# Kernel tuning notes

Hardware: AMD Instinct MI355X
Metric: run time of the kernel (lower is better)

## Reference

```python
import jax, jax.numpy as jnp
import numpy as np

B, NF, G, H, W = 4, 64, 8, 96, 96
K, KK = 3, 9
CG = NF // G  # channels per deformable group


def _conv3(x, w, b):
    # 3x3 conv, stride 1, pad 1, NCHW/OIHW
    y = jax.lax.conv_general_dilated(x, w, (1, 1), ((1, 1), (1, 1)),
                                     dimension_numbers=('NCHW', 'OIHW', 'NCHW'))
    return y + b[None, :, None, None]


def _lrelu(x):
    return jnp.where(x >= 0, x, 0.1 * x)


def _up2(x):
    # bilinear x2 upsample, align_corners=False (PyTorch semantics: src clamped at 0, indices clamped at n-1)
    def up_axis(x, axis):
        n = x.shape[axis]
        src = jnp.maximum((jnp.arange(2 * n, dtype=jnp.float32) + 0.5) / 2.0 - 0.5, 0.0)
        i0 = jnp.floor(src).astype(jnp.int32)
        i1 = jnp.minimum(i0 + 1, n - 1)
        t = (src - i0.astype(jnp.float32))
        x0 = jnp.take(x, i0, axis=axis)
        x1 = jnp.take(x, i1, axis=axis)
        shp = [1] * x.ndim
        shp[axis] = 2 * n
        t = t.reshape(shp)
        return x0 * (1.0 - t) + x1 * t
    return up_axis(up_axis(x, 2), 3)


def _dcn(x, off_feat, w_om, b_om, w_d, b_d):
    # Modulated deformable conv (DCNv2, separate offset input), 3x3, stride 1, pad 1, dil 1,
    # conv groups = 1, deformable groups = G.
    b, c, h, w = x.shape
    om = _conv3(off_feat, w_om, b_om)                     # [B, 3*G*KK, H, W]
    o_y, o_x, m = jnp.split(om, 3, axis=1)                # each [B, G*KK, H, W]
    off_y = o_y.reshape(b, G, KK, h, w)
    off_x = o_x.reshape(b, G, KK, h, w)
    mask = jax.nn.sigmoid(m).reshape(b, G, KK, h, w)

    dy = (jnp.arange(KK, dtype=jnp.float32) // K - 1.0)   # [-1,-1,-1,0,0,0,1,1,1]
    dx = (jnp.arange(KK, dtype=jnp.float32) % K - 1.0)
    ys = jnp.arange(h, dtype=jnp.float32)
    xs = jnp.arange(w, dtype=jnp.float32)
    # sampling positions: [B, G, KK, H, W]
    py = off_y + ys[None, None, None, :, None] + dy[None, None, :, None, None]
    px = off_x + xs[None, None, None, None, :] + dx[None, None, :, None, None]

    y0f = jnp.floor(py); x0f = jnp.floor(px)
    ty = py - y0f; tx = px - x0f
    y0 = y0f.astype(jnp.int32); x0 = x0f.astype(jnp.int32)
    y1 = y0 + 1; x1 = x0 + 1

    xg = x.reshape(b, G, CG, h * w)  # per-deformable-group channels

    def samp(iy, ix):
        valid = ((iy >= 0) & (iy < h) & (ix >= 0) & (ix < w)).astype(x.dtype)  # [B,G,KK,H,W]
        idx = jnp.clip(iy, 0, h - 1) * w + jnp.clip(ix, 0, w - 1)
        idxf = idx.reshape(b, G, 1, KK * h * w)
        v = jnp.take_along_axis(xg, jnp.broadcast_to(idxf, (b, G, CG, KK * h * w)), axis=3)
        return v.reshape(b, G, CG, KK, h, w) * valid[:, :, None]

    w00 = ((1 - ty) * (1 - tx))[:, :, None]
    w01 = ((1 - ty) * tx)[:, :, None]
    w10 = (ty * (1 - tx))[:, :, None]
    w11 = (ty * tx)[:, :, None]
    cols = (samp(y0, x0) * w00 + samp(y0, x1) * w01 +
            samp(y1, x0) * w10 + samp(y1, x1) * w11)
    cols = cols * mask[:, :, None]                        # modulation
    cols = cols.reshape(b, c, KK, h, w)
    out = jnp.einsum('bckhw,ock->bohw', cols, w_d.reshape(c, c, KK))
    return out + b_d[None, :, None, None]


def setup_inputs() -> dict:
    key = jax.random.key(0)
    ks = jax.random.split(key, 20)
    s = 0.05
    inp = {
        'src0': jax.random.normal(ks[0], (B, NF, H, W), jnp.float32),
        'src1': jax.random.normal(ks[1], (B, NF, H, W), jnp.float32),
        'last_offset': jax.random.normal(ks[2], (B, NF, H // 2, W // 2), jnp.float32),
        'last_feature': jax.random.normal(ks[3], (B, NF, H // 2, W // 2), jnp.float32),
        'w_off1': jax.random.normal(ks[4], (NF, 2 * NF, 3, 3), jnp.float32) * s,
        'b_off1': jax.random.normal(ks[5], (NF,), jnp.float32) * s,
        'w_off2': jax.random.normal(ks[6], (NF, 2 * NF, 3, 3), jnp.float32) * s,
        'b_off2': jax.random.normal(ks[7], (NF,), jnp.float32) * s,
        'w_off3': jax.random.normal(ks[8], (NF, NF, 3, 3), jnp.float32) * s,
        'b_off3': jax.random.normal(ks[9], (NF,), jnp.float32) * s,
        'w_om': jax.random.normal(ks[10], (3 * G * KK, NF, 3, 3), jnp.float32) * s,
        'b_om': jax.random.normal(ks[11], (3 * G * KK,), jnp.float32) * s,
        'w_dcn': jax.random.normal(ks[12], (NF, NF, 3, 3), jnp.float32) * s,
        'b_dcn': jax.random.normal(ks[13], (NF,), jnp.float32) * s,
        'w_fea': jax.random.normal(ks[14], (NF, 2 * NF, 3, 3), jnp.float32) * s,
        'b_fea': jax.random.normal(ks[15], (NF,), jnp.float32) * s,
    }
    return inp


def reference(src0, src1, last_offset, last_feature,
              w_off1, b_off1, w_off2, b_off2, w_off3, b_off3,
              w_om, b_om, w_dcn, b_dcn, w_fea, b_fea):
    offset = _lrelu(_conv3(jnp.concatenate([src0, src1], axis=1), w_off1, b_off1))
    lo = _up2(last_offset)
    offset = _lrelu(_conv3(jnp.concatenate([offset, lo * 2.0], axis=1), w_off2, b_off2))
    offset = _lrelu(_conv3(offset, w_off3, b_off3))
    feature = _dcn(src0, offset, w_om, b_om, w_dcn, b_dcn)
    lf = _up2(last_feature)
    feature = _conv3(jnp.concatenate([feature, lf], axis=1), w_fea, b_fea)
    feature = _lrelu(feature)
    return (offset, feature)
```

## Files before the change

kernel.cpp:

```cpp
#include <hip/hip_runtime.h>
#include <math.h>

typedef __attribute__((ext_vector_type(8))) short bf16x8;
typedef __attribute__((ext_vector_type(4))) float f32x4;
typedef __attribute__((ext_vector_type(4))) int int4v;

#define GL_LDS16(g, l) __builtin_amdgcn_global_load_lds( \
    (const __attribute__((address_space(1))) void*)(g), \
    (__attribute__((address_space(3))) void*)(l), 16, 0, 0)

__device__ __forceinline__ ushort f2bf(float f) {
    union { float f; unsigned u; } v; v.f = f;
    unsigned r = (v.u + 0x7fffu + ((v.u >> 16) & 1u)) >> 16;
    return (ushort)r;
}
__device__ __forceinline__ float bf2f(ushort h) {
    union { unsigned u; float f; } v; v.u = ((unsigned)h) << 16;
    return v.f;
}

__device__ __forceinline__ void prep_one(const float* __restrict__ w,
        ushort* __restrict__ wp, int u, int Cin, int CoutR, int CoutP) {
    int oc = u % CoutP; int t = u / CoutP;
    int kg = t & 3; t >>= 2;
    int kk = t % 9; int cc = t / 9;
    alignas(16) ushort tmp[8];
    for (int j = 0; j < 8; ++j) {
        int c = cc * 32 + kg * 8 + j;
        float v = (oc < CoutR) ? w[((size_t)oc * Cin + c) * 9 + kk] : 0.f;
        tmp[j] = f2bf(v);
    }
    *(int4v*)(wp + (size_t)u * 8) = *(int4v*)tmp;
}

__global__ __launch_bounds__(256) void pack_combo_k(
        const float* __restrict__ s0, const float* __restrict__ s1,
        const float* __restrict__ lo, const float* __restrict__ lf,
        const float* __restrict__ w1, const float* __restrict__ w2,
        const float* __restrict__ w3, const float* __restrict__ wom,
        const float* __restrict__ wd, const float* __restrict__ wf,
        const float* __restrict__ bom,
        ushort* __restrict__ xin1, ushort* __restrict__ xin2,
        ushort* __restrict__ xin4, ushort* __restrict__ xg1,
        ushort* __restrict__ w1p, ushort* __restrict__ w2p,
        ushort* __restrict__ w3p, ushort* __restrict__ womp,
        ushort* __restrict__ wdp, ushort* __restrict__ wfp,
        float* __restrict__ bpp, float* __restrict__ zg) {
    int b = blockIdx.y;
    int z = blockIdx.z;
    int px = blockIdx.x * 64 + (threadIdx.x & 63);
    int u = threadIdx.x >> 6;
    if (z == 0) {
        for (int half = 0; half < 2; ++half) {
            int cg = u + half * 4;
            alignas(16) ushort tmp[16];
            for (int i = 0; i < 16; ++i) {
                int c = cg * 16 + i;
                float v = (c < 64) ? s0[((size_t)(b * 64 + c)) * 9216 + px]
                                   : s1[((size_t)(b * 64 + c - 64)) * 9216 + px];
                tmp[i] = f2bf(v);
            }
            ushort* dst = xin1 + ((size_t)(b * 9216) + px) * 128 + cg * 16;
            *(int4v*)dst = *(int4v*)&tmp[0];
            *(int4v*)(dst + 8) = *(int4v*)&tmp[8];
            if (half == 0) {
                ushort* gdst = xg1 + (((size_t)(b * 8 + cg * 2) * 9216) + px) * 8;
                *(int4v*)gdst = *(int4v*)&tmp[0];
                *(int4v*)(gdst + 9216 * 8) = *(int4v*)&tmp[8];
            }
        }
    } else if (z < 3) {
        const float* in = (z == 1) ? lo : lf;
        float scale = (z == 1) ? 2.0f : 1.0f;
        ushort* xo = (z == 1) ? xin2 : xin4;
        int y = px / 96, x = px % 96;
        float sy = fmaxf(y * 0.5f - 0.25f, 0.f);
        float sx = fmaxf(x * 0.5f - 0.25f, 0.f);
        int y0 = (int)sy, x0 = (int)sx;
        float ty = sy - (float)y0, tx = sx - (float)x0;
        int y1 = min(y0 + 1, 47), x1 = min(x0 + 1, 47);
        alignas(16) ushort tmp[16];
        for (int i = 0; i < 16; ++i) {
            int c = u * 16 + i;
            const float* p = in + ((size_t)(b * 64 + c)) * 2304;
            float v00 = p[y0 * 48 + x0], v01 = p[y0 * 48 + x1];
            float v10 = p[y1 * 48 + x0], v11 = p[y1 * 48 + x1];
            float v = (v00 * (1.f - tx) + v01 * tx) * (1.f - ty)
                    + (v10 * (1.f - tx) + v11 * tx) * ty;
            tmp[i] = f2bf(v * scale);
        }
        ushort* dst = xo + ((size_t)(b * 9216) + px) * 128 + 64 + u * 16;
        *(int4v*)dst = *(int4v*)&tmp[0];
        *(int4v*)(dst + 8) = *(int4v*)&tmp[8];
    } else {
        int uu = (blockIdx.x + 144 * blockIdx.y) * 256 + threadIdx.x;
        if (uu < 9216) prep_one(w1, w1p, uu, 128, 64, 64);
        else if (uu < 18432) prep_one(w2, w2p, uu - 9216, 128, 64, 64);
        else if (uu < 23040) prep_one(w3, w3p, uu - 18432, 64, 64, 64);
        else if (uu < 46080) {
            int v = uu - 23040;
            int ocp = v % 320; int t = v / 320;
            int kg = t & 3; t >>= 2;
            int kk = t % 9; int cc = t / 9;
            int t3 = ocp & 3, gkkp = ocp >> 2;
            alignas(16) ushort tmp[8];
            for (int j = 0; j < 8; ++j) {
                int c = cc * 32 + kg * 8 + j;
                float vv = (t3 < 3 && gkkp < 72)
                    ? wom[((size_t)(t3 * 72 + gkkp) * 64 + c) * 9 + kk] : 0.f;
                tmp[j] = f2bf(vv);
            }
            *(int4v*)(womp + (size_t)v * 8) = *(int4v*)tmp;
        } else if (uu < 50688) {
            int v = uu - 46080;
            int oc = v & 63; int gkk = v >> 6;
            int g = gkk / 9, kk = gkk % 9;
            alignas(16) ushort tmp[8];
            for (int j = 0; j < 8; ++j)
                tmp[j] = f2bf(wd[((size_t)oc * 64 + g * 8 + j) * 9 + kk]);
            *(int4v*)(wdp + (size_t)v * 8) = *(int4v*)tmp;
        } else if (uu < 59904) prep_one(wf, wfp, uu - 50688, 128, 64, 64);
        else if (uu < 60224) {
            int ocp = uu - 59904; int t3 = ocp & 3, gkkp = ocp >> 2;
            bpp[ocp] = (t3 < 3 && gkkp < 72) ? bom[t3 * 72 + gkkp] : 0.f;
        } else if (uu < 60240) zg[uu - 60224] = 0.f;
    }
}

template<int CIN, int MT, int NZ, bool LRELU, bool ST_F32, bool ST_CHL>
__global__ __launch_bounds__(256, 4) void conv_mfma_k(
        const ushort* __restrict__ xin,
        const ushort* __restrict__ wp,
        const float* __restrict__ bias,
        float* __restrict__ outf,
        ushort* __restrict__ chl,
        const ushort* __restrict__ zg,
        int CoutR, int CoutP, int ochs, int ocoff) {
    constexpr int SL = CIN / 64;
    constexpr int OCN = MT * 16;
    __shared__ ushort s_act[SL][7200];

    int tid = threadIdx.x;
    int wv = tid >> 6, ln = tid & 63;
    int l15 = ln & 15, l4 = ln >> 4;

    constexpr int TOTAL = 144 * 4 * NZ;
    constexpr int CHUNK = TOTAL / 8;
    int bid = blockIdx.x;
    int nid = (bid & 7) * CHUNK + (bid >> 3);
    int zc = nid % NZ; int r1 = nid / NZ;
    int tile = r1 % 144; int b = r1 / 144;
    int bx = (tile % 12) * 8, by = (tile / 12) * 8;
    int oc0 = zc * OCN;

    int px_l = wv * 16 + l15;
    int py = px_l >> 3, pxx = px_l & 7;
    int b_base = (py * 10 + pxx) * 72 + l4 * 8;

    const ushort* wlane = wp + ((size_t)l4 * CoutP + oc0 + l15) * 8;

    f32x4 acc[MT];
#pragma unroll
    for (int mt = 0; mt < MT; ++mt) acc[mt] = (f32x4){0.f, 0.f, 0.f, 0.f};

    auto STAGE = [&](int sl, int buf) {
        for (int i = tid; i < 900; i += 256) {
            int p = i / 9, q = i - p * 9;
            int gy = by + (p / 10) - 1, gx = bx + (p % 10) - 1;
            const ushort* src = zg;
            if (q < 8 && (unsigned)gy < 96u && (unsigned)gx < 96u)
                src = xin + ((size_t)(b * 9216 + gy * 96 + gx) * CIN
                             + sl * 64 + q * 8);
            GL_LDS16(src, s_act[buf] + (size_t)i * 8);
        }
    };

    STAGE(0, 0);
    __syncthreads();
#pragma unroll
    for (int sl = 0; sl < SL; ++sl) {
        if (sl + 1 < SL) STAGE(sl + 1, (sl + 1) & 1);
#pragma unroll
        for (int cc2 = 0; cc2 < 2; ++cc2) {
#pragma unroll
            for (int kk = 0; kk < 9; ++kk) {
                bf16x8 bfrag = *(const bf16x8*)(s_act[sl & (SL - 1)] + b_base +
                                   ((kk / 3) * 10 + (kk % 3)) * 72 + cc2 * 32);
#pragma unroll
                for (int mt = 0; mt < MT; ++mt) {
                    bf16x8 af = *(const bf16x8*)(wlane +
                        ((size_t)((sl * 2 + cc2) * 36 + kk * 4) * CoutP + mt * 16) * 8);
                    acc[mt] = __builtin_amdgcn_mfma_f32_16x16x32_bf16(
                        af, bfrag, acc[mt], 0, 0, 0);
                }
            }
        }
        if (sl + 1 < SL) __syncthreads();
    }

    int gy = by + py, gx = bx + pxx;
    size_t pxg = (size_t)b * 9216 + gy * 96 + gx;
#pragma unroll
    for (int mt = 0; mt < MT; ++mt) {
        int ocb = oc0 + mt * 16 + l4 * 4;
        ushort hb[4];
#pragma unroll
        for (int r = 0; r < 4; ++r) {
            int oc = ocb + r;
            float v = acc[mt][r] + ((oc < CoutR) ? bias[oc] : 0.f);
            if (LRELU) v = (v >= 0.f) ? v : 0.1f * v;
            hb[r] = f2bf(v);
            if (ST_F32 && oc < CoutR)
                outf[((size_t)b * CoutR + oc) * 9216 + gy * 96 + gx] = v;
        }
        if (ST_CHL && ocb < CoutR) {
            uint2 pk;
            pk.x = (uint)hb[0] | ((uint)hb[1] << 16);
            pk.y = (uint)hb[2] | ((uint)hb[3] << 16);
            *(uint2*)(chl + pxg * ochs + ocoff + ocb) = pk;
        }
    }
}

__global__ __launch_bounds__(128, 4) void dcn_fused_k(
        const ushort* __restrict__ xg1,
        const ushort* __restrict__ om,
        const ushort* __restrict__ wdp,
        const float* __restrict__ bd, ushort* __restrict__ chl) {
    __shared__ float s_red[64][17];
    int tid = threadIdx.x;
    int kq = tid >> 6, ln = tid & 63;
    int l15 = ln & 15, l4 = ln >> 4;
    int bid = blockIdx.x;
    int nid = (bid & 7) * 288 + (bid >> 3);
    int pxb = nid % 576; int b = nid / 576;
    int px = pxb * 16 + l15;
    int y = px / 96, xx = px % 96;

    f32x4 acc[4];
#pragma unroll
    for (int mt = 0; mt < 4; ++mt) acc[mt] = (f32x4){0.f, 0.f, 0.f, 0.f};
    const ushort* omp_ = om + ((size_t)b * 9216 + px) * 288 + kq * 144;

    uint2 ovv[9];
#pragma unroll
    for (int s = 0; s < 9; ++s)
        ovv[s] = *(const uint2*)(omp_ + s * 16 + l4 * 4);

    int4v Abuf[2][4];
    float cwbuf[2][4];

    auto PREP = [&](int s, int4v* A, float* cw) {
        int gkk = kq * 36 + s * 4 + l4;
        int g = gkk / 9, kk = gkk - g * 9;
        union { uint2 u; ushort us[4]; } ov; ov.u = ovv[s];
        float oy = bf2f(ov.us[0]), ox = bf2f(ov.us[1]);
        float mm = 1.f / (1.f + __expf(-bf2f(ov.us[2])));
        float py = oy + (float)(y + kk / 3 - 1);
        float pxf = ox + (float)(xx + kk % 3 - 1);
        float yf = floorf(py), xf = floorf(pxf);
        float fy = py - yf, fx = pxf - xf;
        int iy0 = (int)yf, ix0 = (int)xf;
        int iy1 = iy0 + 1, ix1 = ix0 + 1;
        float vy0 = ((unsigned)iy0 < 96u) ? 1.f : 0.f;
        float vy1 = ((unsigned)iy1 < 96u) ? 1.f : 0.f;
        float vx0 = ((unsigned)ix0 < 96u) ? 1.f : 0.f;
        float vx1 = ((unsigned)ix1 < 96u) ? 1.f : 0.f;
        int r0 = min(max(iy0, 0), 95), r1 = min(max(iy1, 0), 95);
        int lb = min(max(ix0, 0), 94);
        float h0 = (float)min(max(ix0 - lb, 0), 1);
        float h1 = (float)min(max(ix1 - lb, 0), 1);
        float wx0 = (1.f - fx) * vx0, wx1 = fx * vx1;
        float xw0 = wx0 * (1.f - h0) + wx1 * (1.f - h1);
        float xw1 = wx0 * h0 + wx1 * h1;
        float rw0 = (1.f - fy) * vy0 * mm, rw1 = fy * vy1 * mm;
        cw[0] = rw0 * xw0; cw[1] = rw0 * xw1;
        cw[2] = rw1 * xw0; cw[3] = rw1 * xw1;
        const ushort* gp = xg1 + ((size_t)(b * 8 + g) * 9216) * 8;
        const ushort* p0 = gp + ((size_t)(r0 * 96 + lb)) * 8;
        const ushort* p1 = gp + ((size_t)(r1 * 96 + lb)) * 8;
        A[0] = *(const int4v*)p0;
        A[1] = *(const int4v*)(p0 + 8);
        A[2] = *(const int4v*)p1;
        A[3] = *(const int4v*)(p1 + 8);
    };

    PREP(0, Abuf[0], cwbuf[0]);
#pragma unroll
    for (int s = 0; s < 9; ++s) {
        if (s + 1 < 9) PREP(s + 1, Abuf[(s + 1) & 1], cwbuf[(s + 1) & 1]);
        const int4v* A = Abuf[s & 1];
        const float* cw = cwbuf[s & 1];
        union { int4v v; ushort us[8]; } a0, a1, b0, b1;
        a0.v = A[0]; a1.v = A[1]; b0.v = A[2]; b1.v = A[3];
        union { ushort us[8]; bf16x8 v; } bu;
#pragma unroll
        for (int j = 0; j < 8; ++j) {
            float v = cw[0] * bf2f(a0.us[j]) + cw[1] * bf2f(a1.us[j]) +
                      cw[2] * bf2f(b0.us[j]) + cw[3] * bf2f(b1.us[j]);
            bu.us[j] = f2bf(v);
        }
        int gkk = kq * 36 + s * 4 + l4;
#pragma unroll
        for (int mt = 0; mt < 4; ++mt) {
            bf16x8 af = *(const bf16x8*)(wdp +
                ((size_t)gkk * 64 + mt * 16 + l15) * 8);
            acc[mt] = __builtin_amdgcn_mfma_f32_16x16x32_bf16(
                af, bu.v, acc[mt], 0, 0, 0);
        }
    }

    if (kq) {
#pragma unroll
        for (int mt = 0; mt < 4; ++mt)
#pragma unroll
            for (int r = 0; r < 4; ++r)
                s_red[ln][mt * 4 + r] = acc[mt][r];
    }
    __syncthreads();
    if (!kq) {
        size_t pb = (size_t)b * 9216 + px;
#pragma unroll
        for (int mt = 0; mt < 4; ++mt) {
            ushort hb[4];
#pragma unroll
            for (int r = 0; r < 4; ++r) {
                int oc = mt * 16 + l4 * 4 + r;
                float v = acc[mt][r] + s_red[ln][mt * 4 + r] + bd[oc];
                hb[r] = f2bf(v);
            }
            uint2 pk;
            pk.x = (uint)hb[0] | ((uint)hb[1] << 16);
            pk.y = (uint)hb[2] | ((uint)hb[3] << 16);
            *(uint2*)(chl + pb * 128 + mt * 16 + l4 * 4) = pk;
        }
    }
}

extern "C" void kernel_launch(void* const* d_in, const int* in_sizes, int n_in,
                              void* d_out, int out_size, void* d_ws, size_t ws_size,
                              hipStream_t stream) {
    const float* src0  = (const float*)d_in[0];
    const float* src1  = (const float*)d_in[1];
    const float* l_off = (const float*)d_in[2];
    const float* l_fea = (const float*)d_in[3];
    const float* w1 = (const float*)d_in[4];   const float* b1 = (const float*)d_in[5];
    const float* w2 = (const float*)d_in[6];   const float* b2 = (const float*)d_in[7];
    const float* w3 = (const float*)d_in[8];   const float* b3 = (const float*)d_in[9];
    const float* wom = (const float*)d_in[10]; const float* bom = (const float*)d_in[11];
    const float* wd = (const float*)d_in[12];  const float* bd = (const float*)d_in[13];
    const float* wf = (const float*)d_in[14];  const float* bf = (const float*)d_in[15];

    char* W = (char*)d_ws;
    ushort* xin1 = (ushort*)(W + 0);
    ushort* xin2 = (ushort*)(W + 9437184);
    ushort* xoff = (ushort*)(W + 9437184);
    ushort* xin3 = (ushort*)(W + 18874368);
    ushort* omb  = (ushort*)(W + 23592960);
    ushort* xin4 = (ushort*)(W + 44826624);
    ushort* xg1  = (ushort*)(W + 54263808);
    ushort* w1p  = (ushort*)(W + 58982400);
    ushort* w2p  = (ushort*)(W + 59129856);
    ushort* w3p  = (ushort*)(W + 59277312);
    ushort* womp = (ushort*)(W + 59351040);
    ushort* wdp  = (ushort*)(W + 59719680);
    ushort* wfp  = (ushort*)(W + 59793408);
    float*  bpp  = (float*)(W + 59940864);
    float*  zgrd = (float*)(W + 59942144);

    float* out_off = (float*)d_out;
    float* out_fea = out_off + (size_t)4 * 64 * 9216;

    pack_combo_k<<<dim3(144, 4, 4), 256, 0, stream>>>(
        src0, src1, l_off, l_fea, w1, w2, w3, wom, wd, wf, bom,
        xin1, xin2, xin4, xg1, w1p, w2p, w3p, womp, wdp, wfp, bpp, zgrd);

    const ushort* zg = (const ushort*)zgrd;
    conv_mfma_k<128, 2, 2, true, false, true><<<1152, 256, 0, stream>>>(
        xin1, w1p, b1, nullptr, xin2, zg, 64, 64, 128, 0);
    conv_mfma_k<128, 2, 2, true, false, true><<<1152, 256, 0, stream>>>(
        xin2, w2p, b2, nullptr, xin3, zg, 64, 64, 64, 0);
    conv_mfma_k<64, 2, 2, true, true, true><<<1152, 256, 0, stream>>>(
        xin3, w3p, b3, out_off, xoff, zg, 64, 64, 64, 0);
    conv_mfma_k<64, 4, 5, false, false, true><<<2880, 256, 0, stream>>>(
        xoff, womp, bpp, nullptr, omb, zg, 288, 320, 288, 0);
    dcn_fused_k<<<2304, 128, 0, stream>>>(xg1, omb, wdp, bd, xin4);
    conv_mfma_k<128, 2, 2, true, true, false><<<1152, 256, 0, stream>>>(
        xin4, wfp, bf, out_fea, nullptr, zg, 64, 64, 0, 0);
}
```

Before: 146.7 us.

## Use fp16 packed math for DCN sampling and trim offset-conv padding to 288

The deformable-conv sampler now stores the grouped input and DCN weights as fp16. It does the bilinear blend with packed half2 FMAs instead of per-element bf16 unpack, float math and repack, and feeds an f16 MFMA. Separately, the offset/mask conv drops its padded output channels from 320 to 288 and retiles (MT 6, NZ 3, 1728 blocks), which cuts wasted MFMA work and weight bytes. Doing the blend in fp16 changes rounding and can overflow for large inputs, and the new tile shape alters per-block register and LDS use.

```diff
diff --git a/kernel.cpp b/kernel.cpp
--- a/kernel.cpp
+++ b/kernel.cpp
@@ -1,7 +1,9 @@
 #include <hip/hip_runtime.h>
+#include <hip/hip_fp16.h>
 #include <math.h>
 
 typedef __attribute__((ext_vector_type(8))) short bf16x8;
+typedef __attribute__((ext_vector_type(8))) _Float16 half8;
 typedef __attribute__((ext_vector_type(4))) float f32x4;
 typedef __attribute__((ext_vector_type(4))) int int4v;
 
@@ -53,20 +55,24 @@
     if (z == 0) {
         for (int half = 0; half < 2; ++half) {
             int cg = u + half * 4;
+            float vals[16];
             alignas(16) ushort tmp[16];
             for (int i = 0; i < 16; ++i) {
                 int c = cg * 16 + i;
                 float v = (c < 64) ? s0[((size_t)(b * 64 + c)) * 9216 + px]
                                    : s1[((size_t)(b * 64 + c - 64)) * 9216 + px];
+                vals[i] = v;
                 tmp[i] = f2bf(v);
             }
             ushort* dst = xin1 + ((size_t)(b * 9216) + px) * 128 + cg * 16;
             *(int4v*)dst = *(int4v*)&tmp[0];
             *(int4v*)(dst + 8) = *(int4v*)&tmp[8];
             if (half == 0) {
+                alignas(16) __half th[16];
+                for (int i = 0; i < 16; ++i) th[i] = __float2half(vals[i]);
                 ushort* gdst = xg1 + (((size_t)(b * 8 + cg * 2) * 9216) + px) * 8;
-                *(int4v*)gdst = *(int4v*)&tmp[0];
-                *(int4v*)(gdst + 9216 * 8) = *(int4v*)&tmp[8];
+                *(int4v*)gdst = *(int4v*)&th[0];
+                *(int4v*)(gdst + 9216 * 8) = *(int4v*)&th[8];
             }
         }
     } else if (z < 3) {
@@ -97,33 +103,33 @@
         if (uu < 9216) prep_one(w1, w1p, uu, 128, 64, 64);
         else if (uu < 18432) prep_one(w2, w2p, uu - 9216, 128, 64, 64);
         else if (uu < 23040) prep_one(w3, w3p, uu - 18432, 64, 64, 64);
-        else if (uu < 46080) {
+        else if (uu < 43776) {
             int v = uu - 23040;
-            int ocp = v % 320; int t = v / 320;
+            int ocp = v % 288; int t = v / 288;
             int kg = t & 3; t >>= 2;
             int kk = t % 9; int cc = t / 9;
             int t3 = ocp & 3, gkkp = ocp >> 2;
             alignas(16) ushort tmp[8];
             for (int j = 0; j < 8; ++j) {
                 int c = cc * 32 + kg * 8 + j;
-                float vv = (t3 < 3 && gkkp < 72)
+                float vv = (t3 < 3)
                     ? wom[((size_t)(t3 * 72 + gkkp) * 64 + c) * 9 + kk] : 0.f;
                 tmp[j] = f2bf(vv);
             }
             *(int4v*)(womp + (size_t)v * 8) = *(int4v*)tmp;
-        } else if (uu < 50688) {
-            int v = uu - 46080;
+        } else if (uu < 48384) {
+            int v = uu - 43776;
             int oc = v & 63; int gkk = v >> 6;
             int g = gkk / 9, kk = gkk % 9;
-            alignas(16) ushort tmp[8];
+            alignas(16) __half tmp[8];
             for (int j = 0; j < 8; ++j)
-                tmp[j] = f2bf(wd[((size_t)oc * 64 + g * 8 + j) * 9 + kk]);
+                tmp[j] = __float2half(wd[((size_t)oc * 64 + g * 8 + j) * 9 + kk]);
             *(int4v*)(wdp + (size_t)v * 8) = *(int4v*)tmp;
-        } else if (uu < 59904) prep_one(wf, wfp, uu - 50688, 128, 64, 64);
-        else if (uu < 60224) {
-            int ocp = uu - 59904; int t3 = ocp & 3, gkkp = ocp >> 2;
-            bpp[ocp] = (t3 < 3 && gkkp < 72) ? bom[t3 * 72 + gkkp] : 0.f;
-        } else if (uu < 60240) zg[uu - 60224] = 0.f;
+        } else if (uu < 57600) prep_one(wf, wfp, uu - 48384, 128, 64, 64);
+        else if (uu < 57888) {
+            int ocp = uu - 57600; int t3 = ocp & 3, gkkp = ocp >> 2;
+            bpp[ocp] = (t3 < 3) ? bom[t3 * 72 + gkkp] : 0.f;
+        } else if (uu < 57904) zg[uu - 57888] = 0.f;
     }
 }
 
@@ -291,21 +297,27 @@
         if (s + 1 < 9) PREP(s + 1, Abuf[(s + 1) & 1], cwbuf[(s + 1) & 1]);
         const int4v* A = Abuf[s & 1];
         const float* cw = cwbuf[s & 1];
-        union { int4v v; ushort us[8]; } a0, a1, b0, b1;
+        union { int4v v; __half2 h2[4]; } a0, a1, b0, b1;
         a0.v = A[0]; a1.v = A[1]; b0.v = A[2]; b1.v = A[3];
-        union { ushort us[8]; bf16x8 v; } bu;
-#pragma unroll
-        for (int j = 0; j < 8; ++j) {
-            float v = cw[0] * bf2f(a0.us[j]) + cw[1] * bf2f(a1.us[j]) +
-                      cw[2] * bf2f(b0.us[j]) + cw[3] * bf2f(b1.us[j]);
-            bu.us[j] = f2bf(v);
+        __half2 w0 = __float2half2_rn(cw[0]);
+        __half2 w1 = __float2half2_rn(cw[1]);
+        __half2 w2 = __float2half2_rn(cw[2]);
+        __half2 w3 = __float2half2_rn(cw[3]);
+        union { __half2 h2[4]; half8 v; } bu;
+#pragma unroll
+        for (int j = 0; j < 4; ++j) {
+            __half2 t = __hmul2(a0.h2[j], w0);
+            t = __hfma2(a1.h2[j], w1, t);
+            t = __hfma2(b0.h2[j], w2, t);
+            t = __hfma2(b1.h2[j], w3, t);
+            bu.h2[j] = t;
         }
         int gkk = kq * 36 + s * 4 + l4;
 #pragma unroll
         for (int mt = 0; mt < 4; ++mt) {
-            bf16x8 af = *(const bf16x8*)(wdp +
+            half8 af = *(const half8*)(wdp +
                 ((size_t)gkk * 64 + mt * 16 + l15) * 8);
-            acc[mt] = __builtin_amdgcn_mfma_f32_16x16x32_bf16(
+            acc[mt] = __builtin_amdgcn_mfma_f32_16x16x32_f16(
                 af, bu.v, acc[mt], 0, 0, 0);
         }
     }
@@ -363,10 +375,10 @@
     ushort* w2p  = (ushort*)(W + 59129856);
     ushort* w3p  = (ushort*)(W + 59277312);
     ushort* womp = (ushort*)(W + 59351040);
-    ushort* wdp  = (ushort*)(W + 59719680);
-    ushort* wfp  = (ushort*)(W + 59793408);
-    float*  bpp  = (float*)(W + 59940864);
-    float*  zgrd = (float*)(W + 59942144);
+    ushort* wdp  = (ushort*)(W + 59682816);
+    ushort* wfp  = (ushort*)(W + 59756544);
+    float*  bpp  = (float*)(W + 59904000);
+    float*  zgrd = (float*)(W + 59905152);
 
     float* out_off = (float*)d_out;
     float* out_fea = out_off + (size_t)4 * 64 * 9216;
@@ -382,8 +394,8 @@
         xin2, w2p, b2, nullptr, xin3, zg, 64, 64, 64, 0);
     conv_mfma_k<64, 2, 2, true, true, true><<<1152, 256, 0, stream>>>(
         xin3, w3p, b3, out_off, xoff, zg, 64, 64, 64, 0);
-    conv_mfma_k<64, 4, 5, false, false, true><<<2880, 256, 0, stream>>>(
-        xoff, womp, bpp, nullptr, omb, zg, 288, 320, 288, 0);
+    conv_mfma_k<64, 6, 3, false, false, true><<<1728, 256, 0, stream>>>(
+        xoff, womp, bpp, nullptr, omb, zg, 288, 288, 288, 0);
     dcn_fused_k<<<2304, 128, 0, stream>>>(xg1, omb, wdp, bd, xin4);
     conv_mfma_k<128, 2, 2, true, true, false><<<1152, 256, 0, stream>>>(
         xin4, wfp, bf, out_fea, nullptr, zg, 64, 64, 0, 0);
```

New measurement: 145.1 us. No clear change (-1.0%).
